# Optimization experiments

Hardware: AMD Instinct MI355X
Metric: run time of the kernel (lower is better)

The kernel has to match this reference:

```python
import jax, jax.numpy as jnp
import numpy as np

B, T, C = 2, 2048, 2048
NH, NKV, HD = 16, 4, 128
GATE_CH = 12
WINDOW = 1024


def apply_rotary_emb(x, cos, sin):
    # x: (B,T,H,HD); cos/sin: (1,T,1,HD//2)
    d = x.shape[3] // 2
    x1, x2 = x[..., :d], x[..., d:]
    return jnp.concatenate([x1 * cos + x2 * sin, -x1 * sin + x2 * cos], axis=3)


def rms_norm(x):
    return x * jax.lax.rsqrt(jnp.mean(jnp.square(x), axis=-1, keepdims=True) + 1e-06)


def setup_inputs() -> dict:
    key = jax.random.key(0)
    ks = jax.random.split(key, 7)
    # realistic RoPE tables
    theta = 10000.0 ** (-jnp.arange(HD // 2, dtype=jnp.float32) / (HD // 2))
    ang = jnp.arange(T, dtype=jnp.float32)[:, None] * theta[None, :]
    cos = jnp.cos(ang)[None, :, None, :]
    sin = jnp.sin(ang)[None, :, None, :]
    return {
        "x": jax.random.normal(ks[0], (B, T, C), jnp.float32),
        "ve": jax.random.normal(ks[1], (B, T, NKV * HD), jnp.float32),
        "cos": cos,
        "sin": sin,
        "Wq": 0.02 * jax.random.normal(ks[2], (NH * HD, C), jnp.float32),
        "Wk": 0.02 * jax.random.normal(ks[3], (NKV * HD, C), jnp.float32),
        "Wv": 0.02 * jax.random.normal(ks[4], (NKV * HD, C), jnp.float32),
        "Wproj": 0.02 * jax.random.normal(ks[5], (C, C), jnp.float32),
        "Wgate": 0.02 * jax.random.normal(ks[6], (NKV, GATE_CH), jnp.float32),
        "window_size": WINDOW,
    }


def reference(x, ve, cos, sin, Wq, Wk, Wv, Wproj, Wgate, window_size):
    B_, T_, C_ = x.shape
    q = (x @ Wq.T).reshape(B_, T_, NH, HD)
    k = (x @ Wk.T).reshape(B_, T_, NKV, HD)
    v = (x @ Wv.T).reshape(B_, T_, NKV, HD)
    # value-embedding gate-add
    gate = 3.0 * jax.nn.sigmoid(x[..., :GATE_CH] @ Wgate.T)  # (B,T,NKV)
    v = v + gate[..., None] * ve.reshape(B_, T_, NKV, HD)
    # RoPE + QK RMSNorm + scale
    q = rms_norm(apply_rotary_emb(q, cos, sin)) * 1.2
    k = rms_norm(apply_rotary_emb(k, cos, sin)) * 1.2
    # GQA head-repeat
    rep = NH // NKV
    k = jnp.repeat(k, rep, axis=2)
    v = jnp.repeat(v, rep, axis=2)
    # sliding-window causal bias (window_size > 0 branch)
    r = jnp.arange(T_)
    mask = (r[None, :] <= r[:, None]) & (r[:, None] - r[None, :] <= window_size)
    bias = jnp.where(mask, 0.0, jnp.finfo(x.dtype).min)  # (T,T)
    scores = jnp.einsum("bthd,bshd->bhts", q, k) * (1.0 / np.sqrt(HD).astype(np.float32))
    scores = scores + bias[None, None, :, :]
    w = jax.nn.softmax(scores, axis=-1)
    y = jnp.einsum("bhts,bshd->bthd", w, v).reshape(B_, T_, -1)
    return y @ Wproj.T
```

## Files before the change

kernel.cpp:

```cpp
#include <hip/hip_runtime.h>
#include <hip/hip_bf16.h>

#define BB   2
#define TT   2048
#define CC   2048
#define NHq  16
#define NKVq 4
#define HDq  128
#define ROWS (BB*TT)
#define NQKV (NHq*HDq + 2*NKVq*HDq)

using bf16 = __hip_bfloat16;
using short8  = __attribute__((ext_vector_type(8))) short;
using short4v = __attribute__((ext_vector_type(4))) short;
using f32x4   = __attribute__((ext_vector_type(4))) float;

#define MFMA16(a,b,c) __builtin_amdgcn_mfma_f32_16x16x32_bf16((a),(b),(c),0,0,0)

__device__ __forceinline__ void gll16(const bf16* g, void* l) {
    __builtin_amdgcn_global_load_lds((const __attribute__((address_space(1))) void*)g,
                                     (__attribute__((address_space(3))) void*)l,
                                     16, 0, 0);
}

__global__ void cast_all(const float* __restrict__ x,  const float* __restrict__ wq,
                         const float* __restrict__ wk, const float* __restrict__ wv,
                         const float* __restrict__ wp, bf16* __restrict__ dst) {
    long e = ((long)blockIdx.x * 256 + threadIdx.x) * 4;
    const float* src; long off;
    if (e < 8388608L)       { src = x;  off = e; }
    else if (e < 12582912L) { src = wq; off = e - 8388608L; }
    else if (e < 13631488L) { src = wk; off = e - 12582912L; }
    else if (e < 14680064L) { src = wv; off = e - 13631488L; }
    else                    { src = wp; off = e - 14680064L; }
    float4 v = *reinterpret_cast<const float4*>(src + off);
    ushort4 o;
    o.x = __bfloat16_as_ushort(__float2bfloat16(v.x));
    o.y = __bfloat16_as_ushort(__float2bfloat16(v.y));
    o.z = __bfloat16_as_ushort(__float2bfloat16(v.z));
    o.w = __bfloat16_as_ushort(__float2bfloat16(v.w));
    *reinterpret_cast<ushort4*>(dst + e) = o;
}

template<int OUT_F32>
__global__ __launch_bounds__(256) void gemm_bt(const bf16* __restrict__ A,
                                               const bf16* __restrict__ B,
                                               void* __restrict__ Cp,
                                               int M, int N, int K) {
    const int bm = blockIdx.x * 128;
    const int bn = blockIdx.y * 128;
    const int tid = threadIdx.x;
    const int lane = tid & 63;
    const int w = tid >> 6;
    const int wr = w >> 1, wc = w & 1;

    __shared__ __align__(16) bf16 As[128 * 64];
    __shared__ __align__(16) bf16 Bs[128 * 64];

    f32x4 acc[4][4];
#pragma unroll
    for (int i = 0; i < 4; ++i)
#pragma unroll
        for (int j = 0; j < 4; ++j) acc[i][j] = f32x4{0.f, 0.f, 0.f, 0.f};

    const int srow = tid >> 3;
    const int sch  = tid & 7;

    const int fr = lane & 15;
    const int kq = lane >> 4;

    for (int k0 = 0; k0 < K; k0 += 64) {
        __syncthreads();
#pragma unroll
        for (int i = 0; i < 4; ++i) {
            int row = i * 32 + srow;
            int c = sch ^ (row & 7);
            gll16(&A[(size_t)(bm + row) * K + k0 + c * 8], (char*)As + i * 4096 + tid * 16);
            gll16(&B[(size_t)(bn + row) * K + k0 + c * 8], (char*)Bs + i * 4096 + tid * 16);
        }
        __syncthreads();

#pragma unroll
        for (int kk = 0; kk < 2; ++kk) {
            short8 af[4], bfr[4];
#pragma unroll
            for (int m = 0; m < 4; ++m) {
                int r = wr * 64 + m * 16 + fr;
                af[m] = *reinterpret_cast<const short8*>(
                    (const char*)As + r * 128 + (((kk * 4 + kq) ^ (r & 7)) * 16));
            }
#pragma unroll
            for (int n = 0; n < 4; ++n) {
                int r = wc * 64 + n * 16 + fr;
                bfr[n] = *reinterpret_cast<const short8*>(
                    (const char*)Bs + r * 128 + (((kk * 4 + kq) ^ (r & 7)) * 16));
            }
            __builtin_amdgcn_s_setprio(1);
#pragma unroll
            for (int m = 0; m < 4; ++m)
#pragma unroll
                for (int n = 0; n < 4; ++n)
                    acc[m][n] = MFMA16(af[m], bfr[n], acc[m][n]);
            __builtin_amdgcn_s_setprio(0);
        }
    }

    const int cr = (lane >> 4) * 4;
    const int cc = lane & 15;
#pragma unroll
    for (int m = 0; m < 4; ++m)
#pragma unroll
        for (int n = 0; n < 4; ++n) {
            int row = bm + wr * 64 + m * 16 + cr;
            int col = bn + wc * 64 + n * 16 + cc;
#pragma unroll
            for (int j = 0; j < 4; ++j) {
                float v = acc[m][n][j];
                if (OUT_F32) ((float*)Cp)[(size_t)(row + j) * N + col] = v;
                else         ((bf16*)Cp)[(size_t)(row + j) * N + col] = __float2bfloat16(v);
            }
        }
}

__global__ __launch_bounds__(256) void postproc(const float* __restrict__ x,
                                                const float* __restrict__ ve,
                                                const float* __restrict__ cosb,
                                                const float* __restrict__ sinb,
                                                const float* __restrict__ Wgate,
                                                bf16* __restrict__ qkv) {
    const int row = blockIdx.x;
    const int t = row & (TT - 1);
    const int tid = threadIdx.x;
    __shared__ float gate_s[NKVq];
    if (tid < NKVq) {
        float g = 0.f;
#pragma unroll
        for (int c = 0; c < 12; ++c) g += x[(size_t)row * CC + c] * Wgate[tid * 12 + c];
        gate_s[tid] = 3.0f / (1.0f + __expf(-g));
    }
    __syncthreads();

    bf16* qkvr = qkv + (size_t)row * NQKV;

    if (tid < 160) {
        const int hh = tid >> 3, c = tid & 7;
        const int off = (hh < NHq) ? hh * HDq : 2048 + (hh - NHq) * HDq;
        const int d0 = c * 8;
        short8 x1v = *reinterpret_cast<const short8*>(&qkvr[off + d0]);
        short8 x2v = *reinterpret_cast<const short8*>(&qkvr[off + 64 + d0]);
        float4 c0 = *reinterpret_cast<const float4*>(&cosb[(size_t)t * 64 + d0]);
        float4 c1 = *reinterpret_cast<const float4*>(&cosb[(size_t)t * 64 + d0 + 4]);
        float4 s0 = *reinterpret_cast<const float4*>(&sinb[(size_t)t * 64 + d0]);
        float4 s1 = *reinterpret_cast<const float4*>(&sinb[(size_t)t * 64 + d0 + 4]);
        float cv[8] = {c0.x, c0.y, c0.z, c0.w, c1.x, c1.y, c1.z, c1.w};
        float sv[8] = {s0.x, s0.y, s0.z, s0.w, s1.x, s1.y, s1.z, s1.w};
        float r1[8], r2[8], ss = 0.f;
#pragma unroll
        for (int e = 0; e < 8; ++e) {
            float x1 = __bfloat162float(__ushort_as_bfloat16((ushort)x1v[e]));
            float x2 = __bfloat162float(__ushort_as_bfloat16((ushort)x2v[e]));
            r1[e] =  x1 * cv[e] + x2 * sv[e];
            r2[e] = -x1 * sv[e] + x2 * cv[e];
            ss += r1[e] * r1[e] + r2[e] * r2[e];
        }
#pragma unroll
        for (int m = 1; m < 8; m <<= 1) ss += __shfl_xor(ss, m);
        float sc = rsqrtf(ss * (1.0f / 128.0f) + 1e-6f) * 1.2f;
        short8 o1, o2;
#pragma unroll
        for (int e = 0; e < 8; ++e) {
            o1[e] = (short)__bfloat16_as_ushort(__float2bfloat16(r1[e] * sc));
            o2[e] = (short)__bfloat16_as_ushort(__float2bfloat16(r2[e] * sc));
        }
        *reinterpret_cast<short8*>(&qkvr[off + d0])      = o1;
        *reinterpret_cast<short8*>(&qkvr[off + 64 + d0]) = o2;
    } else if (tid < 224) {
        const int u = tid - 160;
        const int e0 = u * 8;
        short8 vv = *reinterpret_cast<const short8*>(&qkvr[2560 + e0]);
        float4 v0 = *reinterpret_cast<const float4*>(&ve[(size_t)row * 512 + e0]);
        float4 v1 = *reinterpret_cast<const float4*>(&ve[(size_t)row * 512 + e0 + 4]);
        float vef[8] = {v0.x, v0.y, v0.z, v0.w, v1.x, v1.y, v1.z, v1.w};
        const float g = gate_s[u >> 4];
        short8 o;
#pragma unroll
        for (int e = 0; e < 8; ++e) {
            float v = __bfloat162float(__ushort_as_bfloat16((ushort)vv[e])) + g * vef[e];
            o[e] = (short)__bfloat16_as_ushort(__float2bfloat16(v));
        }
        *reinterpret_cast<short8*>(&qkvr[2560 + e0]) = o;
    }
}

__global__ __launch_bounds__(256, 2) void attn_mfma(const bf16* __restrict__ qkv,
                                                    bf16* __restrict__ y,
                                                    const int* __restrict__ winp) {
    const int bid = blockIdx.x;
    const int group = bid >> 8, idx = bid & 255;
    const int bh = idx >> 3, jj = idx & 7;
    const int qt = group ? jj : (15 - jj);
    const int h = bh & 15, b = bh >> 4;
    const int t0 = qt * 128;
    const int kvh = h >> 2;
    const int tid = threadIdx.x;
    const int lane = tid & 63;
    const int w = tid >> 6;
    const int window = winp[0];

    __shared__ __align__(16) bf16 Ks[2][64 * 128];
    __shared__ __align__(16) bf16 Vt[2][128 * 64];
    __shared__ __align__(16) bf16 Ps[4][32 * 64];

    const int fr = lane & 15;
    const int kq = (lane >> 4) * 8;
    const int hi = lane >> 4;
    const float scl2 = 0.08838834764831845f * 1.4426950408889634f;
    const float CAP = 24.0f;

    short8 qf[2][4];
#pragma unroll
    for (int mi = 0; mi < 2; ++mi) {
        const bf16* qp = qkv + ((size_t)(b * TT) + t0 + w * 32 + mi * 16 + fr) * NQKV + h * HDq;
#pragma unroll
        for (int c = 0; c < 4; ++c) {
            short8 v = *reinterpret_cast<const short8*>(&qp[c * 32 + kq]);
#pragma unroll
            for (int e = 0; e < 8; ++e) {
                float f = __bfloat162float(__ushort_as_bfloat16((ushort)v[e])) * scl2;
                v[e] = (short)__bfloat16_as_ushort(__float2bfloat16(f));
            }
            qf[mi][c] = v;
        }
    }

    f32x4 acc[2][8];
#pragma unroll
    for (int mi = 0; mi < 2; ++mi)
#pragma unroll
        for (int n = 0; n < 8; ++n) acc[mi][n] = f32x4{0.f, 0.f, 0.f, 0.f};
    float lrow[2][4];
#pragma unroll
    for (int mi = 0; mi < 2; ++mi)
#pragma unroll
        for (int j = 0; j < 4; ++j) lrow[mi][j] = 0.f;

    int s_lo = t0 - window; if (s_lo < 0) s_lo = 0; s_lo &= ~63;
    const int s_end = t0 + 128;

    const bf16* Kg = qkv + (size_t)b * TT * NQKV + 2048 + kvh * HDq;
    const bf16* Vg = Kg + 512;

    const int str = tid >> 4;
    const int sti = tid & 15;
    const int vf  = tid & 15;
    const int vdc = (tid >> 4) * 8;

    short8 vr[4];

#pragma unroll
    for (int p = 0; p < 4; ++p) {
        int row = p * 16 + str;
        int c16 = sti ^ (row & 7);
        gll16(&Kg[(size_t)(s_lo + row) * NQKV + c16 * 8], (char*)Ks[0] + p * 4096 + tid * 16);
    }
#pragma unroll
    for (int i = 0; i < 4; ++i)
        vr[i] = *reinterpret_cast<const short8*>(&Vg[(size_t)(s_lo + 16 * i + vf) * NQKV + vdc]);
#pragma unroll
    for (int j = 0; j < 8; ++j) {
        short4v col;
        col[0] = vr[0][j]; col[1] = vr[1][j]; col[2] = vr[2][j]; col[3] = vr[3][j];
        *reinterpret_cast<short4v*>((char*)Vt[0] + (vdc + j) * 128 + ((8 * vf) ^ (j << 4))) = col;
    }
    __syncthreads();

    int cur = 0;
    for (int sk = s_lo; sk < s_end; sk += 64) {
        const bool hn = (sk + 64 < s_end);

        if (hn) {
#pragma unroll
            for (int p = 0; p < 4; ++p) {
                int row = p * 16 + str;
                int c16 = sti ^ (row & 7);
                gll16(&Kg[(size_t)(sk + 64 + row) * NQKV + c16 * 8],
                      (char*)Ks[cur ^ 1] + p * 4096 + tid * 16);
            }
#pragma unroll
            for (int i = 0; i < 4; ++i)
                vr[i] = *reinterpret_cast<const short8*>(&Vg[(size_t)(sk + 64 + 16 * i + vf) * NQKV + vdc]);
        }

        f32x4 S[2][4];
#pragma unroll
        for (int mi = 0; mi < 2; ++mi)
#pragma unroll
            for (int n = 0; n < 4; ++n) S[mi][n] = f32x4{0.f, 0.f, 0.f, 0.f};
        __builtin_amdgcn_s_setprio(1);
#pragma unroll
        for (int n = 0; n < 4; ++n) {
            int rb = n * 16 + fr;
#pragma unroll
            for (int c = 0; c < 4; ++c) {
                int colb = c * 64 + kq * 2;
                short8 kf = *reinterpret_cast<const short8*>(
                    (const char*)Ks[cur] + rb * 256 + (colb ^ ((rb & 7) << 4)));
                S[0][n] = MFMA16(qf[0][c], kf, S[0][n]);
                S[1][n] = MFMA16(qf[1][c], kf, S[1][n]);
            }
        }
        __builtin_amdgcn_s_setprio(0);

        const int rw0 = t0 + w * 32;
        const bool interior = (sk + 63 <= rw0) && (rw0 + 31 - sk <= window);
#pragma unroll
        for (int mi = 0; mi < 2; ++mi) {
#pragma unroll
            for (int j = 0; j < 4; ++j) {
                const int rl = hi * 4 + j;
                float s0, s1, s2, s3;
                if (interior) {
                    s0 = S[mi][0][j]; s1 = S[mi][1][j];
                    s2 = S[mi][2][j]; s3 = S[mi][3][j];
                } else {
                    const int r = rw0 + mi * 16 + rl;
                    int c0 = sk + fr, c1 = c0 + 16, c2 = c0 + 32, c3 = c0 + 48;
                    s0 = (c0 <= r && r - c0 <= window) ? S[mi][0][j] : -1e30f;
                    s1 = (c1 <= r && r - c1 <= window) ? S[mi][1][j] : -1e30f;
                    s2 = (c2 <= r && r - c2 <= window) ? S[mi][2][j] : -1e30f;
                    s3 = (c3 <= r && r - c3 <= window) ? S[mi][3][j] : -1e30f;
                }
                float p0 = exp2f(s0 - CAP);
                float p1 = exp2f(s1 - CAP);
                float p2 = exp2f(s2 - CAP);
                float p3 = exp2f(s3 - CAP);
                lrow[mi][j] += (p0 + p1) + (p2 + p3);
                short4v pk;
                pk[0] = (short)__bfloat16_as_ushort(__float2bfloat16(p0));
                pk[1] = (short)__bfloat16_as_ushort(__float2bfloat16(p1));
                pk[2] = (short)__bfloat16_as_ushort(__float2bfloat16(p2));
                pk[3] = (short)__bfloat16_as_ushort(__float2bfloat16(p3));
                const int prow = mi * 16 + rl;
                *reinterpret_cast<short4v*>(
                    (char*)Ps + w * 4096 + prow * 128 + ((8 * fr) ^ ((prow & 7) << 4))) = pk;
            }
        }

        if (hn) {
#pragma unroll
            for (int j = 0; j < 8; ++j) {
                short4v col;
                col[0] = vr[0][j]; col[1] = vr[1][j]; col[2] = vr[2][j]; col[3] = vr[3][j];
                *reinterpret_cast<short4v*>((char*)Vt[cur ^ 1] + (vdc + j) * 128 + ((8 * vf) ^ (j << 4))) = col;
            }
        }

        __builtin_amdgcn_s_setprio(1);
#pragma unroll
        for (int c2 = 0; c2 < 2; ++c2) {
            short8 pa0 = *reinterpret_cast<const short8*>(
                (char*)Ps + w * 4096 + fr * 128 + ((c2 * 64 + hi * 16) ^ ((fr & 7) << 4)));
            short8 pa1 = *reinterpret_cast<const short8*>(
                (char*)Ps + w * 4096 + (16 + fr) * 128 + ((c2 * 64 + hi * 16) ^ ((fr & 7) << 4)));
#pragma unroll
            for (int n = 0; n < 8; ++n) {
                short8 vb = *reinterpret_cast<const short8*>(
                    (char*)Vt[cur] + (n * 16 + fr) * 128 + ((c2 * 64 + hi * 16) ^ ((fr & 7) << 4)));
                acc[0][n] = MFMA16(pa0, vb, acc[0][n]);
                acc[1][n] = MFMA16(pa1, vb, acc[1][n]);
            }
        }
        __builtin_amdgcn_s_setprio(0);

        __syncthreads();
        cur ^= 1;
    }

#pragma unroll
    for (int mi = 0; mi < 2; ++mi)
#pragma unroll
        for (int j = 0; j < 4; ++j) {
            float l = lrow[mi][j];
#pragma unroll
            for (int mm = 1; mm < 16; mm <<= 1) l += __shfl_xor(l, mm);
            const int r = t0 + w * 32 + mi * 16 + hi * 4 + j;
            float inv = 1.f / l;
            bf16* yr = y + ((size_t)(b * TT) + r) * CC + h * HDq;
#pragma unroll
            for (int n = 0; n < 8; ++n)
                yr[n * 16 + fr] = __float2bfloat16(acc[mi][n][j] * inv);
        }
}

extern "C" void kernel_launch(void* const* d_in, const int* in_sizes, int n_in,
                              void* d_out, int out_size, void* d_ws, size_t ws_size,
                              hipStream_t stream) {
    const float* x     = (const float*)d_in[0];
    const float* ve    = (const float*)d_in[1];
    const float* cosb  = (const float*)d_in[2];
    const float* sinb  = (const float*)d_in[3];
    const float* Wq    = (const float*)d_in[4];
    const float* Wk    = (const float*)d_in[5];
    const float* Wv    = (const float*)d_in[6];
    const float* Wproj = (const float*)d_in[7];
    const float* Wgate = (const float*)d_in[8];
    const int*   winp  = (const int*)d_in[9];

    bf16* xb     = (bf16*)d_ws;
    bf16* wqkvb  = xb + (size_t)ROWS * CC;
    bf16* wprojb = wqkvb + (size_t)NQKV * CC;
    bf16* qkvb   = wprojb + (size_t)CC * CC;
    bf16* yb     = xb;

    cast_all<<<18432, 256, 0, stream>>>(x, Wq, Wk, Wv, Wproj, xb);

    gemm_bt<0><<<dim3(ROWS / 128, NQKV / 128), 256, 0, stream>>>(xb, wqkvb, qkvb, ROWS, NQKV, CC);

    postproc<<<ROWS, 256, 0, stream>>>(x, ve, cosb, sinb, Wgate, qkvb);

    attn_mfma<<<BB * NHq * (TT / 128), 256, 0, stream>>>(qkvb, yb, winp);

    gemm_bt<1><<<dim3(ROWS / 128, CC / 128), 256, 0, stream>>>(yb, wprojb, d_out, ROWS, CC, CC);
}
```

Before: 176.0 us.

## Split attention key range across two blocks and combine partial outputs

```diff
diff --git a/kernel.cpp b/kernel.cpp
--- a/kernel.cpp
+++ b/kernel.cpp
@@ -192,11 +192,15 @@
     }
 }
 
-__global__ __launch_bounds__(256, 2) void attn_mfma(const bf16* __restrict__ qkv,
-                                                    bf16* __restrict__ y,
-                                                    const int* __restrict__ winp) {
+__global__ __launch_bounds__(256) void attn_split(const bf16* __restrict__ qkv,
+                                                  bf16* __restrict__ O0,
+                                                  bf16* __restrict__ O1,
+                                                  float* __restrict__ lbuf,
+                                                  const int* __restrict__ winp) {
     const int bid = blockIdx.x;
-    const int group = bid >> 8, idx = bid & 255;
+    const int part = bid >> 9;
+    const int inner = bid & 511;
+    const int group = inner >> 8, idx = inner & 255;
     const int bh = idx >> 3, jj = idx & 7;
     const int qt = group ? jj : (15 - jj);
     const int h = bh & 15, b = bh >> 4;
@@ -207,8 +211,8 @@
     const int w = tid >> 6;
     const int window = winp[0];
 
-    __shared__ __align__(16) bf16 Ks[2][64 * 128];
-    __shared__ __align__(16) bf16 Vt[2][128 * 64];
+    __shared__ __align__(16) bf16 Ks[64 * 128];
+    __shared__ __align__(16) bf16 Vt[128 * 64];
     __shared__ __align__(16) bf16 Ps[4][32 * 64];
 
     const int fr = lane & 15;
@@ -245,7 +249,10 @@
         for (int j = 0; j < 4; ++j) lrow[mi][j] = 0.f;
 
     int s_lo = t0 - window; if (s_lo < 0) s_lo = 0; s_lo &= ~63;
-    const int s_end = t0 + 128;
+    const int NT = ((t0 + 128) - s_lo) >> 6;
+    const int halfn = NT >> 1;
+    const int sk0 = part ? s_lo : s_lo + halfn * 64;
+    const int skE = part ? s_lo + halfn * 64 : t0 + 128;
 
     const bf16* Kg = qkv + (size_t)b * TT * NQKV + 2048 + kvh * HDq;
     const bf16* Vg = Kg + 512;
@@ -261,31 +268,23 @@
     for (int p = 0; p < 4; ++p) {
         int row = p * 16 + str;
         int c16 = sti ^ (row & 7);
-        gll16(&Kg[(size_t)(s_lo + row) * NQKV + c16 * 8], (char*)Ks[0] + p * 4096 + tid * 16);
+        gll16(&Kg[(size_t)(sk0 + row) * NQKV + c16 * 8], (char*)Ks + p * 4096 + tid * 16);
     }
 #pragma unroll
     for (int i = 0; i < 4; ++i)
-        vr[i] = *reinterpret_cast<const short8*>(&Vg[(size_t)(s_lo + 16 * i + vf) * NQKV + vdc]);
+        vr[i] = *reinterpret_cast<const short8*>(&Vg[(size_t)(sk0 + 16 * i + vf) * NQKV + vdc]);
 #pragma unroll
     for (int j = 0; j < 8; ++j) {
         short4v col;
         col[0] = vr[0][j]; col[1] = vr[1][j]; col[2] = vr[2][j]; col[3] = vr[3][j];
-        *reinterpret_cast<short4v*>((char*)Vt[0] + (vdc + j) * 128 + ((8 * vf) ^ (j << 4))) = col;
+        *reinterpret_cast<short4v*>((char*)Vt + (vdc + j) * 128 + ((8 * vf) ^ (j << 4))) = col;
     }
     __syncthreads();
 
-    int cur = 0;
-    for (int sk = s_lo; sk < s_end; sk += 64) {
-        const bool hn = (sk + 64 < s_end);
+    for (int sk = sk0; sk < skE; sk += 64) {
+        const bool hn = (sk + 64 < skE);
 
         if (hn) {
-#pragma unroll
-            for (int p = 0; p < 4; ++p) {
-                int row = p * 16 + str;
-                int c16 = sti ^ (row & 7);
-                gll16(&Kg[(size_t)(sk + 64 + row) * NQKV + c16 * 8],
-                      (char*)Ks[cur ^ 1] + p * 4096 + tid * 16);
-            }
 #pragma unroll
             for (int i = 0; i < 4; ++i)
                 vr[i] = *reinterpret_cast<const short8*>(&Vg[(size_t)(sk + 64 + 16 * i + vf) * NQKV + vdc]);
@@ -304,7 +303,7 @@
             for (int c = 0; c < 4; ++c) {
                 int colb = c * 64 + kq * 2;
                 short8 kf = *reinterpret_cast<const short8*>(
-                    (const char*)Ks[cur] + rb * 256 + (colb ^ ((rb & 7) << 4)));
+                    (const char*)Ks + rb * 256 + (colb ^ ((rb & 7) << 4)));
                 S[0][n] = MFMA16(qf[0][c], kf, S[0][n]);
                 S[1][n] = MFMA16(qf[1][c], kf, S[1][n]);
             }
@@ -346,6 +345,239 @@
             }
         }
 
+        __syncthreads();
+
+        if (hn) {
+#pragma unroll
+            for (int p = 0; p < 4; ++p) {
+                int row = p * 16 + str;
+                int c16 = sti ^ (row & 7);
+                gll16(&Kg[(size_t)(sk + 64 + row) * NQKV + c16 * 8], (char*)Ks + p * 4096 + tid * 16);
+            }
+        }
+
+        __builtin_amdgcn_s_setprio(1);
+#pragma unroll
+        for (int c2 = 0; c2 < 2; ++c2) {
+            short8 pa0 = *reinterpret_cast<const short8*>(
+                (char*)Ps + w * 4096 + fr * 128 + ((c2 * 64 + hi * 16) ^ ((fr & 7) << 4)));
+            short8 pa1 = *reinterpret_cast<const short8*>(
+                (char*)Ps + w * 4096 + (16 + fr) * 128 + ((c2 * 64 + hi * 16) ^ ((fr & 7) << 4)));
+#pragma unroll
+            for (int n = 0; n < 8; ++n) {
+                short8 vb = *reinterpret_cast<const short8*>(
+                    (char*)Vt + (n * 16 + fr) * 128 + ((c2 * 64 + hi * 16) ^ ((fr & 7) << 4)));
+                acc[0][n] = MFMA16(pa0, vb, acc[0][n]);
+                acc[1][n] = MFMA16(pa1, vb, acc[1][n]);
+            }
+        }
+        __builtin_amdgcn_s_setprio(0);
+
+        __syncthreads();
+
+        if (hn) {
+#pragma unroll
+            for (int j = 0; j < 8; ++j) {
+                short4v col;
+                col[0] = vr[0][j]; col[1] = vr[1][j]; col[2] = vr[2][j]; col[3] = vr[3][j];
+                *reinterpret_cast<short4v*>((char*)Vt + (vdc + j) * 128 + ((8 * vf) ^ (j << 4))) = col;
+            }
+        }
+    }
+
+    bf16* ob = part ? O1 : O0;
+    float* lb = lbuf + (size_t)part * ROWS * NHq;
+#pragma unroll
+    for (int mi = 0; mi < 2; ++mi)
+#pragma unroll
+        for (int j = 0; j < 4; ++j) {
+            float l = lrow[mi][j];
+#pragma unroll
+            for (int mm = 1; mm < 16; mm <<= 1) l += __shfl_xor(l, mm);
+            const int r = t0 + w * 32 + mi * 16 + hi * 4 + j;
+            bf16* yr = ob + ((size_t)(b * TT) + r) * CC + h * HDq;
+#pragma unroll
+            for (int n = 0; n < 8; ++n)
+                yr[n * 16 + fr] = __float2bfloat16(acc[mi][n][j]);
+            if (fr == 0) lb[((size_t)(b * TT) + r) * NHq + h] = l;
+        }
+}
+
+__global__ __launch_bounds__(256) void attn_combine(bf16* __restrict__ O0,
+                                                    const bf16* __restrict__ O1,
+                                                    const float* __restrict__ lbuf) {
+    const int row = blockIdx.x;
+    const int tid = threadIdx.x;
+    const int h = tid >> 4;
+    const size_t off = (size_t)row * CC + tid * 8;
+    float l = lbuf[(size_t)row * NHq + h] + lbuf[(size_t)ROWS * NHq + (size_t)row * NHq + h];
+    float inv = 1.f / l;
+    short8 a = *reinterpret_cast<const short8*>(O0 + off);
+    short8 c = *reinterpret_cast<const short8*>(O1 + off);
+    short8 o;
+#pragma unroll
+    for (int e = 0; e < 8; ++e) {
+        float fa = __bfloat162float(__ushort_as_bfloat16((ushort)a[e]));
+        float fc = __bfloat162float(__ushort_as_bfloat16((ushort)c[e]));
+        o[e] = (short)__bfloat16_as_ushort(__float2bfloat16((fa + fc) * inv));
+    }
+    *reinterpret_cast<short8*>(O0 + off) = o;
+}
+
+__global__ __launch_bounds__(256, 2) void attn_mfma(const bf16* __restrict__ qkv,
+                                                    bf16* __restrict__ y,
+                                                    const int* __restrict__ winp) {
+    const int bid = blockIdx.x;
+    const int group = bid >> 8, idx = bid & 255;
+    const int bh = idx >> 3, jj = idx & 7;
+    const int qt = group ? jj : (15 - jj);
+    const int h = bh & 15, b = bh >> 4;
+    const int t0 = qt * 128;
+    const int kvh = h >> 2;
+    const int tid = threadIdx.x;
+    const int lane = tid & 63;
+    const int w = tid >> 6;
+    const int window = winp[0];
+
+    __shared__ __align__(16) bf16 Ks[2][64 * 128];
+    __shared__ __align__(16) bf16 Vt[2][128 * 64];
+    __shared__ __align__(16) bf16 Ps[4][32 * 64];
+
+    const int fr = lane & 15;
+    const int kq = (lane >> 4) * 8;
+    const int hi = lane >> 4;
+    const float scl2 = 0.08838834764831845f * 1.4426950408889634f;
+    const float CAP = 24.0f;
+
+    short8 qf[2][4];
+#pragma unroll
+    for (int mi = 0; mi < 2; ++mi) {
+        const bf16* qp = qkv + ((size_t)(b * TT) + t0 + w * 32 + mi * 16 + fr) * NQKV + h * HDq;
+#pragma unroll
+        for (int c = 0; c < 4; ++c) {
+            short8 v = *reinterpret_cast<const short8*>(&qp[c * 32 + kq]);
+#pragma unroll
+            for (int e = 0; e < 8; ++e) {
+                float f = __bfloat162float(__ushort_as_bfloat16((ushort)v[e])) * scl2;
+                v[e] = (short)__bfloat16_as_ushort(__float2bfloat16(f));
+            }
+            qf[mi][c] = v;
+        }
+    }
+
+    f32x4 acc[2][8];
+#pragma unroll
+    for (int mi = 0; mi < 2; ++mi)
+#pragma unroll
+        for (int n = 0; n < 8; ++n) acc[mi][n] = f32x4{0.f, 0.f, 0.f, 0.f};
+    float lrow[2][4];
+#pragma unroll
+    for (int mi = 0; mi < 2; ++mi)
+#pragma unroll
+        for (int j = 0; j < 4; ++j) lrow[mi][j] = 0.f;
+
+    int s_lo = t0 - window; if (s_lo < 0) s_lo = 0; s_lo &= ~63;
+    const int s_end = t0 + 128;
+
+    const bf16* Kg = qkv + (size_t)b * TT * NQKV + 2048 + kvh * HDq;
+    const bf16* Vg = Kg + 512;
+
+    const int str = tid >> 4;
+    const int sti = tid & 15;
+    const int vf  = tid & 15;
+    const int vdc = (tid >> 4) * 8;
+
+    short8 vr[4];
+
+#pragma unroll
+    for (int p = 0; p < 4; ++p) {
+        int row = p * 16 + str;
+        int c16 = sti ^ (row & 7);
+        gll16(&Kg[(size_t)(s_lo + row) * NQKV + c16 * 8], (char*)Ks[0] + p * 4096 + tid * 16);
+    }
+#pragma unroll
+    for (int i = 0; i < 4; ++i)
+        vr[i] = *reinterpret_cast<const short8*>(&Vg[(size_t)(s_lo + 16 * i + vf) * NQKV + vdc]);
+#pragma unroll
+    for (int j = 0; j < 8; ++j) {
+        short4v col;
+        col[0] = vr[0][j]; col[1] = vr[1][j]; col[2] = vr[2][j]; col[3] = vr[3][j];
+        *reinterpret_cast<short4v*>((char*)Vt[0] + (vdc + j) * 128 + ((8 * vf) ^ (j << 4))) = col;
+    }
+    __syncthreads();
+
+    int cur = 0;
+    for (int sk = s_lo; sk < s_end; sk += 64) {
+        const bool hn = (sk + 64 < s_end);
+
+        if (hn) {
+#pragma unroll
+            for (int p = 0; p < 4; ++p) {
+                int row = p * 16 + str;
+                int c16 = sti ^ (row & 7);
+                gll16(&Kg[(size_t)(sk + 64 + row) * NQKV + c16 * 8],
+                      (char*)Ks[cur ^ 1] + p * 4096 + tid * 16);
+            }
+#pragma unroll
+            for (int i = 0; i < 4; ++i)
+                vr[i] = *reinterpret_cast<const short8*>(&Vg[(size_t)(sk + 64 + 16 * i + vf) * NQKV + vdc]);
+        }
+
+        f32x4 S[2][4];
+#pragma unroll
+        for (int mi = 0; mi < 2; ++mi)
+#pragma unroll
+            for (int n = 0; n < 4; ++n) S[mi][n] = f32x4{0.f, 0.f, 0.f, 0.f};
+        __builtin_amdgcn_s_setprio(1);
+#pragma unroll
+        for (int n = 0; n < 4; ++n) {
+            int rb = n * 16 + fr;
+#pragma unroll
+            for (int c = 0; c < 4; ++c) {
+                int colb = c * 64 + kq * 2;
+                short8 kf = *reinterpret_cast<const short8*>(
+                    (const char*)Ks[cur] + rb * 256 + (colb ^ ((rb & 7) << 4)));
+                S[0][n] = MFMA16(qf[0][c], kf, S[0][n]);
+                S[1][n] = MFMA16(qf[1][c], kf, S[1][n]);
+            }
+        }
+        __builtin_amdgcn_s_setprio(0);
+
+        const int rw0 = t0 + w * 32;
+        const bool interior = (sk + 63 <= rw0) && (rw0 + 31 - sk <= window);
+#pragma unroll
+        for (int mi = 0; mi < 2; ++mi) {
+#pragma unroll
+            for (int j = 0; j < 4; ++j) {
+                const int rl = hi * 4 + j;
+                float s0, s1, s2, s3;
+                if (interior) {
+                    s0 = S[mi][0][j]; s1 = S[mi][1][j];
+                    s2 = S[mi][2][j]; s3 = S[mi][3][j];
+                } else {
+                    const int r = rw0 + mi * 16 + rl;
+                    int c0 = sk + fr, c1 = c0 + 16, c2 = c0 + 32, c3 = c0 + 48;
+                    s0 = (c0 <= r && r - c0 <= window) ? S[mi][0][j] : -1e30f;
+                    s1 = (c1 <= r && r - c1 <= window) ? S[mi][1][j] : -1e30f;
+                    s2 = (c2 <= r && r - c2 <= window) ? S[mi][2][j] : -1e30f;
+                    s3 = (c3 <= r && r - c3 <= window) ? S[mi][3][j] : -1e30f;
+                }
+                float p0 = exp2f(s0 - CAP);
+                float p1 = exp2f(s1 - CAP);
+                float p2 = exp2f(s2 - CAP);
+                float p3 = exp2f(s3 - CAP);
+                lrow[mi][j] += (p0 + p1) + (p2 + p3);
+                short4v pk;
+                pk[0] = (short)__bfloat16_as_ushort(__float2bfloat16(p0));
+                pk[1] = (short)__bfloat16_as_ushort(__float2bfloat16(p1));
+                pk[2] = (short)__bfloat16_as_ushort(__float2bfloat16(p2));
+                pk[3] = (short)__bfloat16_as_ushort(__float2bfloat16(p3));
+                const int prow = mi * 16 + rl;
+                *reinterpret_cast<short4v*>(
+                    (char*)Ps + w * 4096 + prow * 128 + ((8 * fr) ^ ((prow & 7) << 4))) = pk;
+            }
+        }
+
         if (hn) {
 #pragma unroll
             for (int j = 0; j < 8; ++j) {
@@ -410,15 +642,27 @@
     bf16* wqkvb  = xb + (size_t)ROWS * CC;
     bf16* wprojb = wqkvb + (size_t)NQKV * CC;
     bf16* qkvb   = wprojb + (size_t)CC * CC;
+    bf16* ybp1   = qkvb + (size_t)ROWS * NQKV;
+    float* lbuf  = (float*)(ybp1 + (size_t)ROWS * CC);
     bf16* yb     = xb;
 
+    const size_t needed = ((size_t)ROWS * CC + (size_t)NQKV * CC + (size_t)CC * CC +
+                           (size_t)ROWS * NQKV + (size_t)ROWS * CC) * 2 +
+                          (size_t)2 * ROWS * NHq * 4;
+    const bool can_split = (ws_size >= needed);
+
     cast_all<<<18432, 256, 0, stream>>>(x, Wq, Wk, Wv, Wproj, xb);
 
     gemm_bt<0><<<dim3(ROWS / 128, NQKV / 128), 256, 0, stream>>>(xb, wqkvb, qkvb, ROWS, NQKV, CC);
 
     postproc<<<ROWS, 256, 0, stream>>>(x, ve, cosb, sinb, Wgate, qkvb);
 
-    attn_mfma<<<BB * NHq * (TT / 128), 256, 0, stream>>>(qkvb, yb, winp);
+    if (can_split) {
+        attn_split<<<2 * BB * NHq * (TT / 128), 256, 0, stream>>>(qkvb, yb, ybp1, lbuf, winp);
+        attn_combine<<<ROWS, 256, 0, stream>>>(yb, ybp1, lbuf);
+    } else {
+        attn_mfma<<<BB * NHq * (TT / 128), 256, 0, stream>>>(qkvb, yb, winp);
+    }
 
     gemm_bt<1><<<dim3(ROWS / 128, CC / 128), 256, 0, stream>>>(yb, wprojb, d_out, ROWS, CC, CC);
 }
```

Result: slower. 233.6 us (+32.7%).
